# Kernel tuning notes

Measured on AMD Instinct MI355X. Metric: run time of the kernel, lower is better.

Reference implementation:

```python
import jax, jax.numpy as jnp
import numpy as np


def setup_inputs() -> dict:
    key = jax.random.key(0)
    k1, k2 = jax.random.split(key)
    x = jax.random.normal(k1, (16, 64, 224, 224), dtype=jnp.float32)
    # conv weight [out=1, in=2, kh=7, kw=7]; init roughly mimics small-normal init
    conv_w = jax.random.normal(k2, (1, 2, 7, 7), dtype=jnp.float32) * 0.01
    conv_b = jnp.zeros((1,), dtype=jnp.float32)
    return {"x": x, "conv_w": conv_w, "conv_b": conv_b}


def reference(x, conv_w, conv_b):
    # channel-wise mean and max -> [B, 2, H, W]
    avg_out = jnp.mean(x, axis=1, keepdims=True)
    max_out = jnp.max(x, axis=1, keepdims=True)
    feat = jnp.concatenate([avg_out, max_out], axis=1)
    # 2->1 channel 7x7 conv, padding 3 (same)
    y = jax.lax.conv_general_dilated(
        feat, conv_w,
        window_strides=(1, 1),
        padding=((3, 3), (3, 3)),
        dimension_numbers=("NCHW", "OIHW", "NCHW"),
    ) + conv_b[None, :, None, None]
    # sigmoid gate broadcast-multiplied back onto x
    return jax.nn.sigmoid(y) * x
```

## Files before the change

kernel.cpp:

```cpp
#include <hip/hip_runtime.h>
#include <math.h>

#define BB 16
#define CC 64
#define HH 224
#define WW 224
#define HWSZ (HH * WW)
#define HW4 (HWSZ / 4)
#define R 7
#define TILES (HH / R)
#define FR (R + 6)
#define FW 240
#define W4 (WW / 4)
#define T 512
#define NBLK (BB * TILES)

typedef float f32x4 __attribute__((ext_vector_type(4)));

__global__ __launch_bounds__(T, 4) void fused_kernel(const float* __restrict__ x,
                                                     const float* __restrict__ cw,
                                                     const float* __restrict__ cb,
                                                     float* __restrict__ out) {
    __shared__ float fa[FR * FW];
    __shared__ float fm[FR * FW];
    __shared__ alignas(16) float gate[R * WW];
    __shared__ float wt[98];

    const int blk0 = blockIdx.x;
    const int blk  = (blk0 & 7) * (NBLK / 8) + (blk0 >> 3);
    const int b    = blk >> 5;
    const int tb   = blk & 31;
    const int h0   = tb * R;
    const int t    = threadIdx.x;

    for (int i = t; i < FR * FW; i += T) { fa[i] = 0.f; fm[i] = 0.f; }
    if (t < 98) wt[t] = cw[t];
    __syncthreads();

    const f32x4* xb = reinterpret_cast<const f32x4*>(x) + (size_t)b * (CC * HW4);
    for (int p = t; p < FR * W4; p += T) {
        int pr = p / W4;
        int pc = p - pr * W4;
        int gh = h0 - 3 + pr;
        if ((unsigned)gh >= (unsigned)HH) continue;
        const f32x4* xp = xb + gh * W4 + pc;
        f32x4 s = {0.f, 0.f, 0.f, 0.f};
        f32x4 m = {-INFINITY, -INFINITY, -INFINITY, -INFINITY};
#pragma unroll 8
        for (int c = 0; c < CC; ++c) {
            f32x4 u = xp[(size_t)c * HW4];
            s += u;
            m[0] = fmaxf(m[0], u[0]); m[1] = fmaxf(m[1], u[1]);
            m[2] = fmaxf(m[2], u[2]); m[3] = fmaxf(m[3], u[3]);
        }
        const float inv = 1.0f / 64.0f;
        int o = pr * FW + 3 + pc * 4;
        fa[o + 0] = s[0] * inv; fa[o + 1] = s[1] * inv;
        fa[o + 2] = s[2] * inv; fa[o + 3] = s[3] * inv;
        fm[o + 0] = m[0]; fm[o + 1] = m[1]; fm[o + 2] = m[2]; fm[o + 3] = m[3];
    }
    __syncthreads();

    const float bias = cb[0];
    for (int p = t; p < R * WW; p += T) {
        int r = p / WW;
        int w = p - r * WW;
        float acc = bias;
#pragma unroll
        for (int kh = 0; kh < 7; ++kh) {
            int ro = (r + kh) * FW + w;
#pragma unroll
            for (int kw = 0; kw < 7; ++kw) {
                acc = fmaf(fa[ro + kw], wt[kh * 7 + kw], acc);
                acc = fmaf(fm[ro + kw], wt[49 + kh * 7 + kw], acc);
            }
        }
        gate[p] = 1.0f / (1.0f + expf(-acc));
    }
    __syncthreads();

    f32x4* ob = reinterpret_cast<f32x4*>(out) + (size_t)b * (CC * HW4);
    const f32x4* g4 = reinterpret_cast<const f32x4*>(gate);
    const int NP = R * W4;
    for (int i = t; i < CC * NP; i += T) {
        int c  = i / NP;
        int p  = i - c * NP;
        int pr = p / W4;
        int pc = p - pr * W4;
        size_t off = (size_t)c * HW4 + (size_t)(h0 + pr) * W4 + pc;
        f32x4 v = xb[off];
        f32x4 g = g4[p];
        v *= g;
        __builtin_nontemporal_store(v, ob + off);
    }
}

extern "C" void kernel_launch(void* const* d_in, const int* in_sizes, int n_in,
                              void* d_out, int out_size, void* d_ws, size_t ws_size,
                              hipStream_t stream) {
    const float* x  = (const float*)d_in[0];
    const float* cw = (const float*)d_in[1];
    const float* cb = (const float*)d_in[2];
    float* out = (float*)d_out;

    fused_kernel<<<NBLK, T, 0, stream>>>(x, cw, cb, out);
}
```

Measured before the change: 378.2 us.

## Split channel reduction into separate kernel writing pooled features to workspace

```diff
diff --git a/kernel.cpp b/kernel.cpp
--- a/kernel.cpp
+++ b/kernel.cpp
@@ -7,20 +7,48 @@
 #define WW 224
 #define HWSZ (HH * WW)
 #define HW4 (HWSZ / 4)
+#define W4 (WW / 4)
 #define R 7
 #define TILES (HH / R)
 #define FR (R + 6)
 #define FW 240
-#define W4 (WW / 4)
 #define T 512
 #define NBLK (BB * TILES)
 
+#define TA 256
+#define NPIX (BB * HW4)
+#define NBLKA (NPIX / TA)
+
 typedef float f32x4 __attribute__((ext_vector_type(4)));
 
-__global__ __launch_bounds__(T, 4) void fused_kernel(const float* __restrict__ x,
-                                                     const float* __restrict__ cw,
-                                                     const float* __restrict__ cb,
-                                                     float* __restrict__ out) {
+__global__ __launch_bounds__(TA) void reduce_kernel(const float* __restrict__ x,
+                                                    float* __restrict__ feat) {
+    const int idx = blockIdx.x * TA + threadIdx.x;
+    const int b   = idx / HW4;
+    const int p   = idx - b * HW4;
+    const f32x4* xp = reinterpret_cast<const f32x4*>(x) + (size_t)b * (CC * HW4) + p;
+
+    f32x4 s = {0.f, 0.f, 0.f, 0.f};
+    f32x4 m = {-INFINITY, -INFINITY, -INFINITY, -INFINITY};
+#pragma unroll 16
+    for (int c = 0; c < CC; ++c) {
+        f32x4 u = xp[(size_t)c * HW4];
+        s += u;
+        m[0] = fmaxf(m[0], u[0]); m[1] = fmaxf(m[1], u[1]);
+        m[2] = fmaxf(m[2], u[2]); m[3] = fmaxf(m[3], u[3]);
+    }
+    const float inv = 1.0f / 64.0f;
+    f32x4* fav = reinterpret_cast<f32x4*>(feat);
+    f32x4* fmx = fav + NPIX;
+    fav[idx] = s * inv;
+    fmx[idx] = m;
+}
+
+__global__ __launch_bounds__(T, 4) void gate_kernel(const float* __restrict__ x,
+                                                    const float* __restrict__ feat,
+                                                    const float* __restrict__ cw,
+                                                    const float* __restrict__ cb,
+                                                    float* __restrict__ out) {
     __shared__ float fa[FR * FW];
     __shared__ float fm[FR * FW];
     __shared__ alignas(16) float gate[R * WW];
@@ -37,27 +65,18 @@
     if (t < 98) wt[t] = cw[t];
     __syncthreads();
 
-    const f32x4* xb = reinterpret_cast<const f32x4*>(x) + (size_t)b * (CC * HW4);
-    for (int p = t; p < FR * W4; p += T) {
+    const f32x4* fav = reinterpret_cast<const f32x4*>(feat) + (size_t)b * HW4;
+    const f32x4* fmx = fav + NPIX;
+    for (int q = t; q < 2 * FR * W4; q += T) {
+        int plane = (q >= FR * W4);
+        int p  = plane ? q - FR * W4 : q;
         int pr = p / W4;
         int pc = p - pr * W4;
         int gh = h0 - 3 + pr;
         if ((unsigned)gh >= (unsigned)HH) continue;
-        const f32x4* xp = xb + gh * W4 + pc;
-        f32x4 s = {0.f, 0.f, 0.f, 0.f};
-        f32x4 m = {-INFINITY, -INFINITY, -INFINITY, -INFINITY};
-#pragma unroll 8
-        for (int c = 0; c < CC; ++c) {
-            f32x4 u = xp[(size_t)c * HW4];
-            s += u;
-            m[0] = fmaxf(m[0], u[0]); m[1] = fmaxf(m[1], u[1]);
-            m[2] = fmaxf(m[2], u[2]); m[3] = fmaxf(m[3], u[3]);
-        }
-        const float inv = 1.0f / 64.0f;
-        int o = pr * FW + 3 + pc * 4;
-        fa[o + 0] = s[0] * inv; fa[o + 1] = s[1] * inv;
-        fa[o + 2] = s[2] * inv; fa[o + 3] = s[3] * inv;
-        fm[o + 0] = m[0]; fm[o + 1] = m[1]; fm[o + 2] = m[2]; fm[o + 3] = m[3];
+        f32x4 u = (plane ? fmx : fav)[gh * W4 + pc];
+        float* dst = (plane ? fm : fa) + pr * FW + 3 + pc * 4;
+        dst[0] = u[0]; dst[1] = u[1]; dst[2] = u[2]; dst[3] = u[3];
     }
     __syncthreads();
 
@@ -79,6 +98,7 @@
     }
     __syncthreads();
 
+    const f32x4* xb = reinterpret_cast<const f32x4*>(x) + (size_t)b * (CC * HW4);
     f32x4* ob = reinterpret_cast<f32x4*>(out) + (size_t)b * (CC * HW4);
     const f32x4* g4 = reinterpret_cast<const f32x4*>(gate);
     const int NP = R * W4;
@@ -101,7 +121,9 @@
     const float* x  = (const float*)d_in[0];
     const float* cw = (const float*)d_in[1];
     const float* cb = (const float*)d_in[2];
-    float* out = (float*)d_out;
+    float* out  = (float*)d_out;
+    float* feat = (float*)d_ws;
 
-    fused_kernel<<<NBLK, T, 0, stream>>>(x, cw, cb, out);
+    reduce_kernel<<<NBLKA, TA, 0, stream>>>(x, feat);
+    gate_kernel<<<NBLK, T, 0, stream>>>(x, feat, cw, cb, out);
 }
```

After: 380.4 us. Within noise of the previous version (+0.6%).
